# Optimization experiments

Measured on AMD Instinct MI355X. Metric: run time of the kernel, lower is better.

The kernel has to match this reference:

```python
import jax, jax.numpy as jnp
import numpy as np

H = 128  # hidden_dim
COORD_CLAMP = 100.0


def _glorot(key, shape):
    fan_in, fan_out = shape[0], shape[1]
    lim = float(np.sqrt(6.0 / (fan_in + fan_out)))
    return jax.random.uniform(key, shape, jnp.float32, -lim, lim)


def setup_inputs() -> dict:
    key = jax.random.key(0)
    ks = jax.random.split(key, 20)
    B, N = 2, 512
    inp = {
        "h": jax.random.normal(ks[0], (B, N, H), jnp.float32),
        "pos": jax.random.normal(ks[1], (B, N, 3), jnp.float32),
        "vel": jax.random.normal(ks[2], (B, N, 3), jnp.float32),
        # edge_mlp: Linear(2H+2 -> H), SiLU, Linear(H -> H), SiLU
        "We1": _glorot(ks[3], (2 * H + 2, H)), "be1": jnp.zeros((H,), jnp.float32),
        "We2": _glorot(ks[4], (H, H)), "be2": jnp.zeros((H,), jnp.float32),
        # attention_mlp: Linear(H -> 1), Sigmoid
        "Wa": _glorot(ks[5], (H, 1)), "ba": jnp.zeros((1,), jnp.float32),
        # pos_mlp: Linear(H -> H), SiLU, Linear(H -> 1, no bias)
        "Wp1": _glorot(ks[6], (H, H)), "bp1": jnp.zeros((H,), jnp.float32),
        "Wp2": _glorot(ks[7], (H, 1)),
        # vel_mlp: Linear(H -> H), SiLU, Linear(H -> 1, no bias)
        "Wv1": _glorot(ks[8], (H, H)), "bv1": jnp.zeros((H,), jnp.float32),
        "Wv2": _glorot(ks[9], (H, 1)),
        # node_mlp: Linear(2H -> H), SiLU, Linear(H -> H)
        "Wn1": _glorot(ks[10], (2 * H, H)), "bn1": jnp.zeros((H,), jnp.float32),
        "Wn2": _glorot(ks[11], (H, H)), "bn2": jnp.zeros((H,), jnp.float32),
    }
    return inp


def reference(h, pos, vel, We1, be1, We2, be2, Wa, ba,
              Wp1, bp1, Wp2, Wv1, bv1, Wv2, Wn1, bn1, Wn2, bn2):
    B, N, _ = pos.shape
    # pairwise diffs: [B, N, N, 3]
    pos_diff = pos[:, :, None, :] - pos[:, None, :, :]
    vel_diff = vel[:, :, None, :] - vel[:, None, :, :]
    pos_dist_sq = jnp.sum(pos_diff ** 2, axis=-1, keepdims=True)  # [B,N,N,1]
    vel_dist_sq = jnp.sum(vel_diff ** 2, axis=-1, keepdims=True)
    h_i = jnp.broadcast_to(h[:, :, None, :], (B, N, N, H))
    h_j = jnp.broadcast_to(h[:, None, :, :], (B, N, N, H))
    edge_input = jnp.concatenate([h_i, h_j, pos_dist_sq, vel_dist_sq], axis=-1)  # [B,N,N,2H+2]
    # edge MLP
    m = jax.nn.silu(jnp.einsum('bijc,ch->bijh', edge_input, We1) + be1)
    m_ij = jax.nn.silu(jnp.einsum('bijh,hk->bijk', m, We2) + be2)
    # attention gate
    att = jax.nn.sigmoid(jnp.einsum('bijh,ho->bijo', m_ij, Wa) + ba)  # [B,N,N,1]
    m_ij = m_ij * att
    # tanh-weighted coordinate/velocity updates
    pos_w = jnp.tanh(jnp.einsum('bijh,ho->bijo', jax.nn.silu(jnp.einsum('bijh,hk->bijk', m_ij, Wp1) + bp1), Wp2))
    vel_w = jnp.tanh(jnp.einsum('bijh,ho->bijo', jax.nn.silu(jnp.einsum('bijh,hk->bijk', m_ij, Wv1) + bv1), Wv2))
    denom = jnp.float32(max(N - 1, 1))
    pos_update = jnp.sum(pos_diff * pos_w, axis=2) / denom  # [B,N,3]
    vel_update = jnp.sum(vel_diff * vel_w, axis=2) / denom
    pos_out = jnp.clip(pos + pos_update, -COORD_CLAMP, COORD_CLAMP)
    vel_out = jnp.clip(vel + vel_update, -COORD_CLAMP, COORD_CLAMP)
    # node update
    m_agg = jnp.sum(m_ij, axis=2)  # [B,N,H]
    node_input = jnp.concatenate([h, m_agg], axis=-1)  # [B,N,2H]
    h_out = jax.nn.silu(jnp.einsum('bnc,ch->bnh', node_input, Wn1) + bn1)
    h_out = jnp.einsum('bnh,hk->bnk', h_out, Wn2) + bn2
    h_out = h + h_out  # residual
    return (h_out, pos_out, vel_out)
```

## Files before the change

kernel.cpp:

```cpp
#include <hip/hip_runtime.h>
#include <hip/hip_bf16.h>

#define Hd 128
#define Nn 512
#define TJ 32
#define LSTRIDE 136

typedef __bf16 bf16x8 __attribute__((ext_vector_type(8)));
typedef __bf16 bf16x4 __attribute__((ext_vector_type(4)));
typedef float  floatx4 __attribute__((ext_vector_type(4)));

__device__ __forceinline__ float frcp(float x){ return __builtin_amdgcn_rcpf(x); }
__device__ __forceinline__ float fsilu(float x){ return x * frcp(1.f + __expf(-x)); }
__device__ __forceinline__ float fsigm(float x){ return frcp(1.f + __expf(-x)); }
__device__ __forceinline__ float ftanh(float x){ return 1.f - 2.f * frcp(__expf(2.f*x) + 1.f); }
__device__ __forceinline__ float rfl(float x){
  return __int_as_float(__builtin_amdgcn_readfirstlane(__float_as_int(x)));
}

__global__ __launch_bounds__(256) void prep(const float* __restrict__ h,
                                            const float* __restrict__ We1,
                                            const float* __restrict__ be1,
                                            const float* __restrict__ We2,
                                            const float* __restrict__ Wp1,
                                            const float* __restrict__ Wv1,
                                            float* __restrict__ A,
                                            float* __restrict__ Bm,
                                            __bf16* __restrict__ dst,
                                            float* __restrict__ zbase){
  if (blockIdx.x < 256){
    const int r0 = blockIdx.x * 4;
    const int k = threadIdx.x & 127, ch = threadIdx.x >> 7;
    __shared__ float hL[4][Hd];
    __shared__ float pa[2][4][Hd], pb[2][4][Hd];
    for (int idx = threadIdx.x; idx < 4*Hd; idx += 256)
      hL[idx >> 7][idx & 127] = h[r0*Hd + idx];
    __syncthreads();
    float a[4] = {0.f,0.f,0.f,0.f}, bb[4] = {0.f,0.f,0.f,0.f};
    const int cbase = ch*64;
    #pragma unroll 4
    for (int cc = 0; cc < 64; ++cc){
      const int c = cbase + cc;
      const float wa = We1[c*Hd + k];
      const float wb = We1[(c + Hd)*Hd + k];
      #pragma unroll
      for (int rr = 0; rr < 4; ++rr){
        a[rr]  += hL[rr][c] * wa;
        bb[rr] += hL[rr][c] * wb;
      }
    }
    #pragma unroll
    for (int rr = 0; rr < 4; ++rr){ pa[ch][rr][k] = a[rr]; pb[ch][rr][k] = bb[rr]; }
    __syncthreads();
    if (threadIdx.x < Hd){
      const float be = be1[k];
      #pragma unroll
      for (int rr = 0; rr < 4; ++rr){
        A[(r0+rr)*Hd + k]  = pa[0][rr][k] + pa[1][rr][k] + be;
        Bm[(r0+rr)*Hd + k] = pb[0][rr][k] + pb[1][rr][k];
      }
    }
  } else if (blockIdx.x < 280){
    const int blk = blockIdx.x - 256;
    const int which = blk >> 3, m = blk & 7;
    const float* src = (which == 0) ? We2 : (which == 1 ? Wp1 : Wv1);
    __bf16* d = dst + which * (Hd*Hd);
    #pragma unroll
    for (int it = 0; it < 8; ++it){
      const int sidx = m*2048 + it*256 + threadIdx.x;
      const int kk = sidx >> 7, cc = sidx & 127;
      const int s = kk >> 5, j = kk & 7;
      const int lane = ((kk >> 3) & 3)*16 + (cc & 15);
      const int n = cc >> 4;
      d[n*2048 + s*512 + lane*8 + j] = (__bf16)src[sidx];
    }
  } else {
    const int t0 = (blockIdx.x - 280)*256 + threadIdx.x;
    for (int idx = t0; idx < 137216; idx += 2048) zbase[idx] = 0.f;
  }
}

__device__ __forceinline__ void gemm_kloopT(const __bf16* __restrict__ buf,
                                            const bf16x8* __restrict__ Ws,
                                            int w, int lane, int q, int l15,
                                            floatx4 acc[2][2]){
  const floatx4 zero = {0.f, 0.f, 0.f, 0.f};
  #pragma unroll
  for (int m = 0; m < 2; ++m){ acc[m][0] = zero; acc[m][1] = zero; }
  #pragma unroll
  for (int s = 0; s < 4; ++s){
    bf16x8 bf[2];
    #pragma unroll
    for (int n = 0; n < 2; ++n)
      bf[n] = *(const bf16x8*)&buf[(16*n + l15)*LSTRIDE + s*32 + q*8];
    const bf16x8 a0 = Ws[((2*w + 0)*4 + s)*64 + lane];
    const bf16x8 a1 = Ws[((2*w + 1)*4 + s)*64 + lane];
    #pragma unroll
    for (int n = 0; n < 2; ++n){
      acc[0][n] = __builtin_amdgcn_mfma_f32_16x16x32_bf16(a0, bf[n], acc[0][n], 0, 0, 0);
      acc[1][n] = __builtin_amdgcn_mfma_f32_16x16x32_bf16(a1, bf[n], acc[1][n], 0, 0, 0);
    }
  }
}

__device__ __forceinline__ void wdotT(floatx4 acc[2][2], float att0, float att1,
                                      const float* __restrict__ biasL,
                                      const float* __restrict__ w2L,
                                      int w, int lane, int q, int l15,
                                      float (*part)[TJ]){
  const int fb0 = 32*w + 4*q, fb1 = fb0 + 16;
  const floatx4 bb0 = *(const floatx4*)&biasL[fb0];
  const floatx4 bb1 = *(const floatx4*)&biasL[fb1];
  const floatx4 w0  = *(const floatx4*)&w2L[fb0];
  const floatx4 w1  = *(const floatx4*)&w2L[fb1];
  float p0 = 0.f, p1 = 0.f;
  #pragma unroll
  for (int r = 0; r < 4; ++r){
    p0 += fsilu(fmaf(att0, acc[0][0][r], bb0[r])) * w0[r];
    p0 += fsilu(fmaf(att0, acc[1][0][r], bb1[r])) * w1[r];
    p1 += fsilu(fmaf(att1, acc[0][1][r], bb0[r])) * w0[r];
    p1 += fsilu(fmaf(att1, acc[1][1][r], bb1[r])) * w1[r];
  }
  p0 += __shfl_xor(p0, 16, 64); p0 += __shfl_xor(p0, 32, 64);
  p1 += __shfl_xor(p1, 16, 64); p1 += __shfl_xor(p1, 32, 64);
  if (lane < 16){
    part[w][l15]      = p0;
    part[w][16 + l15] = p1;
  }
}

__global__ __launch_bounds__(256) void egnn_main(
    const float* __restrict__ pos, const float* __restrict__ vel,
    const float* __restrict__ We1, const float* __restrict__ be2,
    const float* __restrict__ Wa,  const float* __restrict__ ba,
    const float* __restrict__ bp1, const float* __restrict__ Wp2,
    const float* __restrict__ bv1, const float* __restrict__ Wv2,
    const float* __restrict__ A,   const float* __restrict__ Bm,
    const __bf16* __restrict__ Wsw,
    float* __restrict__ magg, float* __restrict__ posu, float* __restrict__ velu){

  const int t    = threadIdx.x;
  const int w    = t >> 6;
  const int lane = t & 63;
  const int q    = lane >> 4;
  const int l15  = lane & 15;
  const int node = blockIdx.x >> 1;
  const int half = blockIdx.x & 1;
  const int b    = node >> 9;

  __shared__ float AiL[Hd], wpL[Hd], wvL[Hd];
  __shared__ float be2L[Hd], bp1L[Hd], bv1L[Hd], WaL[Hd], Wp2L[Hd], Wv2L[Hd];
  __shared__ __align__(16) __bf16 bufm [TJ*LSTRIDE];
  __shared__ __align__(16) __bf16 bufij[TJ*LSTRIDE];
  __shared__ float partAtt[4][TJ], partP[4][TJ], partV[4][TJ];
  __shared__ float attL[TJ];

  if (t < Hd){
    AiL[t]  = A[node*Hd + t];
    wpL[t]  = We1[256*Hd + t];
    wvL[t]  = We1[257*Hd + t];
    be2L[t] = be2[t]; bp1L[t] = bp1[t]; bv1L[t] = bv1[t];
    WaL[t]  = Wa[t];  Wp2L[t] = Wp2[t]; Wv2L[t] = Wv2[t];
  }
  const float baV = ba[0];
  const float* pi = &pos[(size_t)node*3];
  const float* vi = &vel[(size_t)node*3];
  const float px = rfl(pi[0]), py = rfl(pi[1]), pz = rfl(pi[2]);
  const float ux = rfl(vi[0]), uy = rfl(vi[1]), uz = rfl(vi[2]);
  __syncthreads();

  const bf16x8* We2s = (const bf16x8*)(Wsw);
  const bf16x8* Wp1s = (const bf16x8*)(Wsw + Hd*Hd);
  const bf16x8* Wv1s = (const bf16x8*)(Wsw + 2*Hd*Hd);

  float accR[8];
  #pragma unroll
  for (int e = 0; e < 8; ++e) accR[e] = 0.f;

  for (int jt = 0; jt < (Nn/2)/TJ; ++jt){
    const int j0 = half*(Nn/2) + jt * TJ;

    {
      const int g  = t & 15;
      const int j2 = t >> 4;
      const floatx4 a0 = *(const floatx4*)&AiL[g*8];
      const floatx4 a1 = *(const floatx4*)&AiL[g*8 + 4];
      const floatx4 p0 = *(const floatx4*)&wpL[g*8];
      const floatx4 p1 = *(const floatx4*)&wpL[g*8 + 4];
      const floatx4 v0 = *(const floatx4*)&wvL[g*8];
      const floatx4 v1 = *(const floatx4*)&wvL[g*8 + 4];
      #pragma unroll
      for (int rr = 0; rr < 2; ++rr){
        const int j = j2 + rr*16;
        const int jg = j0 + j;
        const float* pj = &pos[(size_t)(b*Nn + jg)*3];
        const float* vj = &vel[(size_t)(b*Nn + jg)*3];
        const float dx = px - pj[0], dy = py - pj[1], dz = pz - pj[2];
        const float dp = dx*dx + dy*dy + dz*dz;
        const float ex = ux - vj[0], ey = uy - vj[1], ez = uz - vj[2];
        const float dv = ex*ex + ey*ey + ez*ez;
        const floatx4* Bp4 = (const floatx4*)&Bm[((size_t)(b*Nn + jg))*Hd + g*8];
        const floatx4 b0 = Bp4[0], b1 = Bp4[1];
        union { bf16x8 v; __hip_bfloat162 h2[4]; } o;
        float x[8];
        #pragma unroll
        for (int e = 0; e < 4; ++e){
          x[e]   = fsilu(a0[e] + b0[e] + dp*p0[e] + dv*v0[e]);
          x[4+e] = fsilu(a1[e] + b1[e] + dp*p1[e] + dv*v1[e]);
        }
        o.h2[0] = __float22bfloat162_rn(make_float2(x[0], x[1]));
        o.h2[1] = __float22bfloat162_rn(make_float2(x[2], x[3]));
        o.h2[2] = __float22bfloat162_rn(make_float2(x[4], x[5]));
        o.h2[3] = __float22bfloat162_rn(make_float2(x[6], x[7]));
        *(bf16x8*)&bufm[j*LSTRIDE + g*8] = o.v;
      }
    }
    __syncthreads();

    {
      floatx4 acc[2][2];
      gemm_kloopT(bufm, We2s, w, lane, q, l15, acc);
      const int fb0 = 32*w + 4*q, fb1 = fb0 + 16;
      const floatx4 be0 = *(const floatx4*)&be2L[fb0];
      const floatx4 be1 = *(const floatx4*)&be2L[fb1];
      const floatx4 wa0 = *(const floatx4*)&WaL[fb0];
      const floatx4 wa1 = *(const floatx4*)&WaL[fb1];
      float aw[2];
      #pragma unroll
      for (int n = 0; n < 2; ++n){
        const int j = 16*n + l15;
        float s0[4], s1[4];
        #pragma unroll
        for (int r = 0; r < 4; ++r){
          s0[r] = fsilu(acc[0][n][r] + be0[r]);
          s1[r] = fsilu(acc[1][n][r] + be1[r]);
        }
        aw[n] = s0[0]*wa0[0] + s0[1]*wa0[1] + s0[2]*wa0[2] + s0[3]*wa0[3]
              + s1[0]*wa1[0] + s1[1]*wa1[1] + s1[2]*wa1[2] + s1[3]*wa1[3];
        union { bf16x4 v; __hip_bfloat162 h2[2]; } p0k, p1k;
        p0k.h2[0] = __float22bfloat162_rn(make_float2(s0[0], s0[1]));
        p0k.h2[1] = __float22bfloat162_rn(make_float2(s0[2], s0[3]));
        p1k.h2[0] = __float22bfloat162_rn(make_float2(s1[0], s1[1]));
        p1k.h2[1] = __float22bfloat162_rn(make_float2(s1[2], s1[3]));
        *(bf16x4*)&bufij[j*LSTRIDE + fb0] = p0k.v;
        *(bf16x4*)&bufij[j*LSTRIDE + fb1] = p1k.v;
      }
      aw[0] += __shfl_xor(aw[0], 16, 64); aw[0] += __shfl_xor(aw[0], 32, 64);
      aw[1] += __shfl_xor(aw[1], 16, 64); aw[1] += __shfl_xor(aw[1], 32, 64);
      if (lane < 16){
        partAtt[w][l15]      = aw[0];
        partAtt[w][16 + l15] = aw[1];
      }
    }
    __syncthreads();

    {
      const float att0 = fsigm(partAtt[0][l15] + partAtt[1][l15] +
                               partAtt[2][l15] + partAtt[3][l15] + baV);
      const float att1 = fsigm(partAtt[0][16+l15] + partAtt[1][16+l15] +
                               partAtt[2][16+l15] + partAtt[3][16+l15] + baV);
      if (w == 0 && lane < 16){ attL[l15] = att0; attL[16 + l15] = att1; }
      floatx4 acc[2][2];
      gemm_kloopT(bufij, Wp1s, w, lane, q, l15, acc);
      wdotT(acc, att0, att1, bp1L, Wp2L, w, lane, q, l15, partP);
      gemm_kloopT(bufij, Wv1s, w, lane, q, l15, acc);
      wdotT(acc, att0, att1, bv1L, Wv2L, w, lane, q, l15, partV);
    }
    __syncthreads();

    if (w == 0){
      if (lane < TJ){
        const int jg = j0 + lane;
        const float* pj = &pos[(size_t)(b*Nn + jg)*3];
        const float s4 = partP[0][lane] + partP[1][lane] + partP[2][lane] + partP[3][lane];
        const float pw = ftanh(s4);
        accR[0] += (px - pj[0]) * pw;
        accR[1] += (py - pj[1]) * pw;
        accR[2] += (pz - pj[2]) * pw;
      }
    } else if (w == 1){
      if (lane < TJ){
        const int jg = j0 + lane;
        const float* vj = &vel[(size_t)(b*Nn + jg)*3];
        const float s4 = partV[0][lane] + partV[1][lane] + partV[2][lane] + partV[3][lane];
        const float vw = ftanh(s4);
        accR[0] += (ux - vj[0]) * vw;
        accR[1] += (uy - vj[1]) * vw;
        accR[2] += (uz - vj[2]) * vw;
      }
    } else {
      const int sg   = (w - 2)*8 + (lane & 7);
      const int jsub = lane >> 3;
      #pragma unroll
      for (int jj = 0; jj < 4; ++jj){
        const int j = jj*8 + jsub;
        const float aj = attL[j];
        const bf16x8 v = *(const bf16x8*)&bufij[j*LSTRIDE + sg*8];
        #pragma unroll
        for (int e = 0; e < 8; ++e) accR[e] += aj * (float)v[e];
      }
    }
  }

  if (w == 0 || w == 1){
    float v0 = accR[0], v1 = accR[1], v2 = accR[2];
    #pragma unroll
    for (int off = 1; off < 64; off <<= 1){
      v0 += __shfl_xor(v0, off, 64);
      v1 += __shfl_xor(v1, off, 64);
      v2 += __shfl_xor(v2, off, 64);
    }
    if (lane == 0){
      float* dst = (w == 0) ? &posu[node*3] : &velu[node*3];
      atomicAdd(&dst[0], v0);
      atomicAdd(&dst[1], v1);
      atomicAdd(&dst[2], v2);
    }
  } else {
    const int sg = (w - 2)*8 + (lane & 7);
    #pragma unroll
    for (int off = 8; off < 64; off <<= 1){
      #pragma unroll
      for (int e = 0; e < 8; ++e) accR[e] += __shfl_xor(accR[e], off, 64);
    }
    if ((lane >> 3) == 0){
      #pragma unroll
      for (int e = 0; e < 8; ++e)
        atomicAdd(&magg[node*Hd + sg*8 + e], accR[e]);
    }
  }
}

__global__ __launch_bounds__(256) void egnn_final(
    const float* __restrict__ h, const float* __restrict__ pos, const float* __restrict__ vel,
    const float* __restrict__ Wn1, const float* __restrict__ bn1,
    const float* __restrict__ Wn2, const float* __restrict__ bn2,
    const float* __restrict__ magg, const float* __restrict__ posu,
    const float* __restrict__ velu, float* __restrict__ out){
  const int row = blockIdx.x;
  const int t = threadIdx.x;
  const int k = t & 127, ch = t >> 7;
  __shared__ float ni[2*Hd];
  __shared__ float p1[2][Hd], t1[Hd];
  ni[t] = (t < Hd) ? h[row*Hd + t] : magg[row*Hd + (t - Hd)];
  __syncthreads();
  {
    float a0=0.f,a1=0.f,a2=0.f,a3=0.f;
    const int cb = ch*Hd;
    #pragma unroll 8
    for (int cc = 0; cc < Hd; cc += 4){
      a0 += ni[cb+cc+0] * Wn1[(cb+cc+0)*Hd + k];
      a1 += ni[cb+cc+1] * Wn1[(cb+cc+1)*Hd + k];
      a2 += ni[cb+cc+2] * Wn1[(cb+cc+2)*Hd + k];
      a3 += ni[cb+cc+3] * Wn1[(cb+cc+3)*Hd + k];
    }
    p1[ch][k] = (a0+a1)+(a2+a3);
  }
  __syncthreads();
  if (t < Hd) t1[t] = fsilu(p1[0][t] + p1[1][t] + bn1[t]);
  __syncthreads();
  {
    float a0=0.f,a1=0.f,a2=0.f,a3=0.f;
    const int cb = ch*64;
    #pragma unroll 8
    for (int cc = 0; cc < 64; cc += 4){
      a0 += t1[cb+cc+0] * Wn2[(cb+cc+0)*Hd + k];
      a1 += t1[cb+cc+1] * Wn2[(cb+cc+1)*Hd + k];
      a2 += t1[cb+cc+2] * Wn2[(cb+cc+2)*Hd + k];
      a3 += t1[cb+cc+3] * Wn2[(cb+cc+3)*Hd + k];
    }
    p1[ch][k] = (a0+a1)+(a2+a3);
  }
  __syncthreads();
  if (t < Hd){
    out[row*Hd + t] = ni[t] + p1[0][t] + p1[1][t] + bn2[t];
  } else if (t < Hd + 3){
    const int d = t - Hd;
    const float v = pos[row*3 + d] + posu[row*3 + d] * (1.f/511.f);
    out[2*Nn*Hd + row*3 + d] = fminf(fmaxf(v, -100.f), 100.f);
  } else if (t < Hd + 6){
    const int d = t - Hd - 3;
    const float v = vel[row*3 + d] + velu[row*3 + d] * (1.f/511.f);
    out[2*Nn*Hd + 2*Nn*3 + row*3 + d] = fminf(fmaxf(v, -100.f), 100.f);
  }
}

extern "C" void kernel_launch(void* const* d_in, const int* in_sizes, int n_in,
                              void* d_out, int out_size, void* d_ws, size_t ws_size,
                              hipStream_t stream){
  const float* h   = (const float*)d_in[0];
  const float* pos = (const float*)d_in[1];
  const float* vel = (const float*)d_in[2];
  const float* We1 = (const float*)d_in[3];
  const float* be1 = (const float*)d_in[4];
  const float* We2 = (const float*)d_in[5];
  const float* be2 = (const float*)d_in[6];
  const float* Wa  = (const float*)d_in[7];
  const float* ba  = (const float*)d_in[8];
  const float* Wp1 = (const float*)d_in[9];
  const float* bp1 = (const float*)d_in[10];
  const float* Wp2 = (const float*)d_in[11];
  const float* Wv1 = (const float*)d_in[12];
  const float* bv1 = (const float*)d_in[13];
  const float* Wv2 = (const float*)d_in[14];
  const float* Wn1 = (const float*)d_in[15];
  const float* bn1 = (const float*)d_in[16];
  const float* Wn2 = (const float*)d_in[17];
  const float* bn2 = (const float*)d_in[18];

  float* ws = (float*)d_ws;
  float*  A    = ws;
  float*  Bmm  = ws + 131072;
  float*  magg = ws + 262144;
  float*  posu = ws + 393216;
  float*  velu = ws + 396288;
  __bf16* Wsw  = (__bf16*)(ws + 399360);

  prep      <<<dim3(288),  dim3(256), 0, stream>>>(h, We1, be1, We2, Wp1, Wv1,
                                                   A, Bmm, Wsw, magg);
  egnn_main <<<dim3(2048), dim3(256), 0, stream>>>(pos, vel, We1, be2, Wa, ba, bp1, Wp2,
                                                   bv1, Wv2, A, Bmm, Wsw, magg, posu, velu);
  egnn_final<<<dim3(1024), dim3(256), 0, stream>>>(h, pos, vel, Wn1, bn1, Wn2, bn2,
                                                   magg, posu, velu, (float*)d_out);
}
```

Baseline: 233.4 us.

## Fuse prep, edge and node kernels into one cooperative kernel with grid sync

Replaces the three-kernel pipeline with a single cooperative kernel. Each block handles one node: it computes its own A/B projections and part of the weight swizzle, then runs a grid-wide sync. After that it processes all 512 neighbours instead of half, and performs the node MLP and the position and velocity outputs in place, with no global accumulation buffers. This removes two launches, the zero-fill, and the atomic or global round trips, but halves the grid to 1024 blocks (less parallelism) and adds a grid barrier. The old path stays as a fallback when occupancy is below 4 blocks per CU.

```diff
diff --git a/kernel.cpp b/kernel.cpp
--- a/kernel.cpp
+++ b/kernel.cpp
@@ -1,5 +1,8 @@
 #include <hip/hip_runtime.h>
 #include <hip/hip_bf16.h>
+#include <hip/hip_cooperative_groups.h>
+
+namespace cg = cooperative_groups;
 
 #define Hd 128
 #define Nn 512
@@ -16,68 +19,6 @@
 __device__ __forceinline__ float ftanh(float x){ return 1.f - 2.f * frcp(__expf(2.f*x) + 1.f); }
 __device__ __forceinline__ float rfl(float x){
   return __int_as_float(__builtin_amdgcn_readfirstlane(__float_as_int(x)));
-}
-
-__global__ __launch_bounds__(256) void prep(const float* __restrict__ h,
-                                            const float* __restrict__ We1,
-                                            const float* __restrict__ be1,
-                                            const float* __restrict__ We2,
-                                            const float* __restrict__ Wp1,
-                                            const float* __restrict__ Wv1,
-                                            float* __restrict__ A,
-                                            float* __restrict__ Bm,
-                                            __bf16* __restrict__ dst,
-                                            float* __restrict__ zbase){
-  if (blockIdx.x < 256){
-    const int r0 = blockIdx.x * 4;
-    const int k = threadIdx.x & 127, ch = threadIdx.x >> 7;
-    __shared__ float hL[4][Hd];
-    __shared__ float pa[2][4][Hd], pb[2][4][Hd];
-    for (int idx = threadIdx.x; idx < 4*Hd; idx += 256)
-      hL[idx >> 7][idx & 127] = h[r0*Hd + idx];
-    __syncthreads();
-    float a[4] = {0.f,0.f,0.f,0.f}, bb[4] = {0.f,0.f,0.f,0.f};
-    const int cbase = ch*64;
-    #pragma unroll 4
-    for (int cc = 0; cc < 64; ++cc){
-      const int c = cbase + cc;
-      const float wa = We1[c*Hd + k];
-      const float wb = We1[(c + Hd)*Hd + k];
-      #pragma unroll
-      for (int rr = 0; rr < 4; ++rr){
-        a[rr]  += hL[rr][c] * wa;
-        bb[rr] += hL[rr][c] * wb;
-      }
-    }
-    #pragma unroll
-    for (int rr = 0; rr < 4; ++rr){ pa[ch][rr][k] = a[rr]; pb[ch][rr][k] = bb[rr]; }
-    __syncthreads();
-    if (threadIdx.x < Hd){
-      const float be = be1[k];
-      #pragma unroll
-      for (int rr = 0; rr < 4; ++rr){
-        A[(r0+rr)*Hd + k]  = pa[0][rr][k] + pa[1][rr][k] + be;
-        Bm[(r0+rr)*Hd + k] = pb[0][rr][k] + pb[1][rr][k];
-      }
-    }
-  } else if (blockIdx.x < 280){
-    const int blk = blockIdx.x - 256;
-    const int which = blk >> 3, m = blk & 7;
-    const float* src = (which == 0) ? We2 : (which == 1 ? Wp1 : Wv1);
-    __bf16* d = dst + which * (Hd*Hd);
-    #pragma unroll
-    for (int it = 0; it < 8; ++it){
-      const int sidx = m*2048 + it*256 + threadIdx.x;
-      const int kk = sidx >> 7, cc = sidx & 127;
-      const int s = kk >> 5, j = kk & 7;
-      const int lane = ((kk >> 3) & 3)*16 + (cc & 15);
-      const int n = cc >> 4;
-      d[n*2048 + s*512 + lane*8 + j] = (__bf16)src[sidx];
-    }
-  } else {
-    const int t0 = (blockIdx.x - 280)*256 + threadIdx.x;
-    for (int idx = t0; idx < 137216; idx += 2048) zbase[idx] = 0.f;
-  }
 }
 
 __device__ __forceinline__ void gemm_kloopT(const __bf16* __restrict__ buf,
@@ -129,23 +70,27 @@
   }
 }
 
-__global__ __launch_bounds__(256) void egnn_main(
+__global__ __launch_bounds__(256) void egnn_coop(
+    const float* __restrict__ h,
     const float* __restrict__ pos, const float* __restrict__ vel,
-    const float* __restrict__ We1, const float* __restrict__ be2,
+    const float* __restrict__ We1, const float* __restrict__ be1,
+    const float* __restrict__ be2,
     const float* __restrict__ Wa,  const float* __restrict__ ba,
     const float* __restrict__ bp1, const float* __restrict__ Wp2,
     const float* __restrict__ bv1, const float* __restrict__ Wv2,
-    const float* __restrict__ A,   const float* __restrict__ Bm,
-    const __bf16* __restrict__ Wsw,
-    float* __restrict__ magg, float* __restrict__ posu, float* __restrict__ velu){
+    const float* __restrict__ Wn1, const float* __restrict__ bn1,
+    const float* __restrict__ Wn2, const float* __restrict__ bn2,
+    const float* __restrict__ We2, const float* __restrict__ Wp1,
+    const float* __restrict__ Wv1,
+    float* __restrict__ Bm, __bf16* __restrict__ Wsw,
+    float* __restrict__ out){
 
   const int t    = threadIdx.x;
   const int w    = t >> 6;
   const int lane = t & 63;
   const int q    = lane >> 4;
   const int l15  = lane & 15;
-  const int node = blockIdx.x >> 1;
-  const int half = blockIdx.x & 1;
+  const int node = blockIdx.x;
   const int b    = node >> 9;
 
   __shared__ float AiL[Hd], wpL[Hd], wvL[Hd];
@@ -155,8 +100,47 @@
   __shared__ float partAtt[4][TJ], partP[4][TJ], partV[4][TJ];
   __shared__ float attL[TJ];
 
+  {
+    const int k = t & 127, ch = t >> 7;
+    if (t < Hd) AiL[t] = h[(size_t)node*Hd + t];
+    __syncthreads();
+    float a = 0.f, bm = 0.f;
+    const int cb = ch*64;
+    #pragma unroll 4
+    for (int cc = 0; cc < 64; ++cc){
+      const int c = cb + cc;
+      const float hv = AiL[c];
+      a  += hv * We1[c*Hd + k];
+      bm += hv * We1[(c + Hd)*Hd + k];
+    }
+    float* pa = (float*)bufm;
+    float* pb = pa + 256;
+    pa[ch*128 + k] = a;
+    pb[ch*128 + k] = bm;
+    __syncthreads();
+    if (t < Hd){
+      const float av = pa[t] + pa[128 + t] + be1[t];
+      Bm[(size_t)node*Hd + t] = pb[t] + pb[128 + t];
+      AiL[t] = av;
+    }
+    if (node < 24){
+      const int which = node >> 3, m = node & 7;
+      const float* src = (which == 0) ? We2 : (which == 1 ? Wp1 : Wv1);
+      __bf16* d = Wsw + which * (Hd*Hd);
+      #pragma unroll
+      for (int it = 0; it < 8; ++it){
+        const int sidx = m*2048 + it*256 + t;
+        const int kk = sidx >> 7, cc2 = sidx & 127;
+        const int s = kk >> 5, j = kk & 7;
+        const int ln = ((kk >> 3) & 3)*16 + (cc2 & 15);
+        const int n = cc2 >> 4;
+        d[n*2048 + s*512 + ln*8 + j] = (__bf16)src[sidx];
+      }
+    }
+  }
+  cg::this_grid().sync();
+
   if (t < Hd){
-    AiL[t]  = A[node*Hd + t];
     wpL[t]  = We1[256*Hd + t];
     wvL[t]  = We1[257*Hd + t];
     be2L[t] = be2[t]; bp1L[t] = bp1[t]; bv1L[t] = bv1[t];
@@ -177,8 +161,8 @@
   #pragma unroll
   for (int e = 0; e < 8; ++e) accR[e] = 0.f;
 
-  for (int jt = 0; jt < (Nn/2)/TJ; ++jt){
-    const int j0 = half*(Nn/2) + jt * TJ;
+  for (int jt = 0; jt < Nn/TJ; ++jt){
+    const int j0 = jt * TJ;
 
     {
       const int g  = t & 15;
@@ -222,7 +206,7 @@
       gemm_kloopT(bufm, We2s, w, lane, q, l15, acc);
       const int fb0 = 32*w + 4*q, fb1 = fb0 + 16;
       const floatx4 be0 = *(const floatx4*)&be2L[fb0];
-      const floatx4 be1 = *(const floatx4*)&be2L[fb1];
+      const floatx4 be1v = *(const floatx4*)&be2L[fb1];
       const floatx4 wa0 = *(const floatx4*)&WaL[fb0];
       const floatx4 wa1 = *(const floatx4*)&WaL[fb1];
       float aw[2];
@@ -233,7 +217,7 @@
         #pragma unroll
         for (int r = 0; r < 4; ++r){
           s0[r] = fsilu(acc[0][n][r] + be0[r]);
-          s1[r] = fsilu(acc[1][n][r] + be1[r]);
+          s1[r] = fsilu(acc[1][n][r] + be1v[r]);
         }
         aw[n] = s0[0]*wa0[0] + s0[1]*wa0[1] + s0[2]*wa0[2] + s0[3]*wa0[3]
               + s1[0]*wa1[0] + s1[1]*wa1[1] + s1[2]*wa1[2] + s1[3]*wa1[3];
@@ -268,6 +252,310 @@
     }
     __syncthreads();
 
+    if (w == 0){
+      if (lane < TJ){
+        const int jg = j0 + lane;
+        const float* pj = &pos[(size_t)(b*Nn + jg)*3];
+        const float s4 = partP[0][lane] + partP[1][lane] + partP[2][lane] + partP[3][lane];
+        const float pw = ftanh(s4);
+        accR[0] += (px - pj[0]) * pw;
+        accR[1] += (py - pj[1]) * pw;
+        accR[2] += (pz - pj[2]) * pw;
+      }
+    } else if (w == 1){
+      if (lane < TJ){
+        const int jg = j0 + lane;
+        const float* vj = &vel[(size_t)(b*Nn + jg)*3];
+        const float s4 = partV[0][lane] + partV[1][lane] + partV[2][lane] + partV[3][lane];
+        const float vw = ftanh(s4);
+        accR[0] += (ux - vj[0]) * vw;
+        accR[1] += (uy - vj[1]) * vw;
+        accR[2] += (uz - vj[2]) * vw;
+      }
+    } else {
+      const int sg   = (w - 2)*8 + (lane & 7);
+      const int jsub = lane >> 3;
+      #pragma unroll
+      for (int jj = 0; jj < 4; ++jj){
+        const int j = jj*8 + jsub;
+        const float aj = attL[j];
+        const bf16x8 v = *(const bf16x8*)&bufij[j*LSTRIDE + sg*8];
+        #pragma unroll
+        for (int e = 0; e < 8; ++e) accR[e] += aj * (float)v[e];
+      }
+    }
+  }
+
+  float* sF = (float*)bufm;
+  if (t < Hd) sF[t] = h[(size_t)node*Hd + t];
+
+  if (w == 0 || w == 1){
+    float v0 = accR[0], v1 = accR[1], v2 = accR[2];
+    #pragma unroll
+    for (int off = 1; off < 64; off <<= 1){
+      v0 += __shfl_xor(v0, off, 64);
+      v1 += __shfl_xor(v1, off, 64);
+      v2 += __shfl_xor(v2, off, 64);
+    }
+    if (lane == 0){
+      const float inv = 1.f / 511.f;
+      if (w == 0){
+        float o0 = pi[0] + v0*inv, o1 = pi[1] + v1*inv, o2 = pi[2] + v2*inv;
+        out[2*Nn*Hd + node*3 + 0] = fminf(fmaxf(o0, -100.f), 100.f);
+        out[2*Nn*Hd + node*3 + 1] = fminf(fmaxf(o1, -100.f), 100.f);
+        out[2*Nn*Hd + node*3 + 2] = fminf(fmaxf(o2, -100.f), 100.f);
+      } else {
+        float o0 = vi[0] + v0*inv, o1 = vi[1] + v1*inv, o2 = vi[2] + v2*inv;
+        out[2*Nn*Hd + 2*Nn*3 + node*3 + 0] = fminf(fmaxf(o0, -100.f), 100.f);
+        out[2*Nn*Hd + 2*Nn*3 + node*3 + 1] = fminf(fmaxf(o1, -100.f), 100.f);
+        out[2*Nn*Hd + 2*Nn*3 + node*3 + 2] = fminf(fmaxf(o2, -100.f), 100.f);
+      }
+    }
+  } else {
+    const int sg = (w - 2)*8 + (lane & 7);
+    #pragma unroll
+    for (int off = 8; off < 64; off <<= 1){
+      #pragma unroll
+      for (int e = 0; e < 8; ++e) accR[e] += __shfl_xor(accR[e], off, 64);
+    }
+    if ((lane >> 3) == 0){
+      *(float4*)&sF[128 + sg*8 + 0] = make_float4(accR[0], accR[1], accR[2], accR[3]);
+      *(float4*)&sF[128 + sg*8 + 4] = make_float4(accR[4], accR[5], accR[6], accR[7]);
+    }
+  }
+  __syncthreads();
+
+  {
+    const int k = t & 127, ch = t >> 7;
+    const int cb = ch*Hd;
+    float a0=0.f,a1=0.f,a2=0.f,a3=0.f;
+    #pragma unroll 8
+    for (int cc = 0; cc < Hd; cc += 4){
+      a0 += sF[cb+cc+0] * Wn1[(cb+cc+0)*Hd + k];
+      a1 += sF[cb+cc+1] * Wn1[(cb+cc+1)*Hd + k];
+      a2 += sF[cb+cc+2] * Wn1[(cb+cc+2)*Hd + k];
+      a3 += sF[cb+cc+3] * Wn1[(cb+cc+3)*Hd + k];
+    }
+    sF[256 + ch*128 + k] = (a0+a1)+(a2+a3);
+  }
+  __syncthreads();
+  if (t < Hd) sF[512 + t] = fsilu(sF[256 + t] + sF[384 + t] + bn1[t]);
+  __syncthreads();
+  {
+    const int k = t & 127, ch = t >> 7;
+    const int cb = ch*64;
+    float a0=0.f,a1=0.f,a2=0.f,a3=0.f;
+    #pragma unroll 8
+    for (int cc = 0; cc < 64; cc += 4){
+      a0 += sF[512+cb+cc+0] * Wn2[(cb+cc+0)*Hd + k];
+      a1 += sF[512+cb+cc+1] * Wn2[(cb+cc+1)*Hd + k];
+      a2 += sF[512+cb+cc+2] * Wn2[(cb+cc+2)*Hd + k];
+      a3 += sF[512+cb+cc+3] * Wn2[(cb+cc+3)*Hd + k];
+    }
+    sF[256 + ch*128 + k] = (a0+a1)+(a2+a3);
+  }
+  __syncthreads();
+  if (t < Hd)
+    out[(size_t)node*Hd + t] = sF[t] + sF[256 + t] + sF[384 + t] + bn2[t];
+}
+
+__global__ __launch_bounds__(256) void prep(const float* __restrict__ h,
+                                            const float* __restrict__ We1,
+                                            const float* __restrict__ be1,
+                                            const float* __restrict__ We2,
+                                            const float* __restrict__ Wp1,
+                                            const float* __restrict__ Wv1,
+                                            float* __restrict__ A,
+                                            float* __restrict__ Bm,
+                                            __bf16* __restrict__ dst,
+                                            float* __restrict__ zbase){
+  if (blockIdx.x < 256){
+    const int r0 = blockIdx.x * 4;
+    const int k = threadIdx.x & 127, ch = threadIdx.x >> 7;
+    __shared__ float hL[4][Hd];
+    __shared__ float pa[2][4][Hd], pb[2][4][Hd];
+    for (int idx = threadIdx.x; idx < 4*Hd; idx += 256)
+      hL[idx >> 7][idx & 127] = h[r0*Hd + idx];
+    __syncthreads();
+    float a[4] = {0.f,0.f,0.f,0.f}, bb[4] = {0.f,0.f,0.f,0.f};
+    const int cbase = ch*64;
+    #pragma unroll 4
+    for (int cc = 0; cc < 64; ++cc){
+      const int c = cbase + cc;
+      const float wa = We1[c*Hd + k];
+      const float wb = We1[(c + Hd)*Hd + k];
+      #pragma unroll
+      for (int rr = 0; rr < 4; ++rr){
+        a[rr]  += hL[rr][c] * wa;
+        bb[rr] += hL[rr][c] * wb;
+      }
+    }
+    #pragma unroll
+    for (int rr = 0; rr < 4; ++rr){ pa[ch][rr][k] = a[rr]; pb[ch][rr][k] = bb[rr]; }
+    __syncthreads();
+    if (threadIdx.x < Hd){
+      const float be = be1[k];
+      #pragma unroll
+      for (int rr = 0; rr < 4; ++rr){
+        A[(r0+rr)*Hd + k]  = pa[0][rr][k] + pa[1][rr][k] + be;
+        Bm[(r0+rr)*Hd + k] = pb[0][rr][k] + pb[1][rr][k];
+      }
+    }
+  } else if (blockIdx.x < 280){
+    const int blk = blockIdx.x - 256;
+    const int which = blk >> 3, m = blk & 7;
+    const float* src = (which == 0) ? We2 : (which == 1 ? Wp1 : Wv1);
+    __bf16* d = dst + which * (Hd*Hd);
+    #pragma unroll
+    for (int it = 0; it < 8; ++it){
+      const int sidx = m*2048 + it*256 + threadIdx.x;
+      const int kk = sidx >> 7, cc = sidx & 127;
+      const int s = kk >> 5, j = kk & 7;
+      const int lane = ((kk >> 3) & 3)*16 + (cc & 15);
+      const int n = cc >> 4;
+      d[n*2048 + s*512 + lane*8 + j] = (__bf16)src[sidx];
+    }
+  } else {
+    const int t0 = (blockIdx.x - 280)*256 + threadIdx.x;
+    for (int idx = t0; idx < 137216; idx += 2048) zbase[idx] = 0.f;
+  }
+}
+
+__global__ __launch_bounds__(256) void egnn_main(
+    const float* __restrict__ pos, const float* __restrict__ vel,
+    const float* __restrict__ We1, const float* __restrict__ be2,
+    const float* __restrict__ Wa,  const float* __restrict__ ba,
+    const float* __restrict__ bp1, const float* __restrict__ Wp2,
+    const float* __restrict__ bv1, const float* __restrict__ Wv2,
+    const float* __restrict__ A,   const float* __restrict__ Bm,
+    const __bf16* __restrict__ Wsw,
+    float* __restrict__ magg, float* __restrict__ posu, float* __restrict__ velu){
+
+  const int t    = threadIdx.x;
+  const int w    = t >> 6;
+  const int lane = t & 63;
+  const int q    = lane >> 4;
+  const int l15  = lane & 15;
+  const int node = blockIdx.x >> 1;
+  const int half = blockIdx.x & 1;
+  const int b    = node >> 9;
+
+  __shared__ float AiL[Hd], wpL[Hd], wvL[Hd];
+  __shared__ float be2L[Hd], bp1L[Hd], bv1L[Hd], WaL[Hd], Wp2L[Hd], Wv2L[Hd];
+  __shared__ __align__(16) __bf16 bufm [TJ*LSTRIDE];
+  __shared__ __align__(16) __bf16 bufij[TJ*LSTRIDE];
+  __shared__ float partAtt[4][TJ], partP[4][TJ], partV[4][TJ];
+  __shared__ float attL[TJ];
+
+  if (t < Hd){
+    AiL[t]  = A[node*Hd + t];
+    wpL[t]  = We1[256*Hd + t];
+    wvL[t]  = We1[257*Hd + t];
+    be2L[t] = be2[t]; bp1L[t] = bp1[t]; bv1L[t] = bv1[t];
+    WaL[t]  = Wa[t];  Wp2L[t] = Wp2[t]; Wv2L[t] = Wv2[t];
+  }
+  const float baV = ba[0];
+  const float* pi = &pos[(size_t)node*3];
+  const float* vi = &vel[(size_t)node*3];
+  const float px = rfl(pi[0]), py = rfl(pi[1]), pz = rfl(pi[2]);
+  const float ux = rfl(vi[0]), uy = rfl(vi[1]), uz = rfl(vi[2]);
+  __syncthreads();
+
+  const bf16x8* We2s = (const bf16x8*)(Wsw);
+  const bf16x8* Wp1s = (const bf16x8*)(Wsw + Hd*Hd);
+  const bf16x8* Wv1s = (const bf16x8*)(Wsw + 2*Hd*Hd);
+
+  float accR[8];
+  #pragma unroll
+  for (int e = 0; e < 8; ++e) accR[e] = 0.f;
+
+  for (int jt = 0; jt < (Nn/2)/TJ; ++jt){
+    const int j0 = half*(Nn/2) + jt * TJ;
+    {
+      const int g  = t & 15;
+      const int j2 = t >> 4;
+      const floatx4 a0 = *(const floatx4*)&AiL[g*8];
+      const floatx4 a1 = *(const floatx4*)&AiL[g*8 + 4];
+      const floatx4 p0 = *(const floatx4*)&wpL[g*8];
+      const floatx4 p1 = *(const floatx4*)&wpL[g*8 + 4];
+      const floatx4 v0 = *(const floatx4*)&wvL[g*8];
+      const floatx4 v1 = *(const floatx4*)&wvL[g*8 + 4];
+      #pragma unroll
+      for (int rr = 0; rr < 2; ++rr){
+        const int j = j2 + rr*16;
+        const int jg = j0 + j;
+        const float* pj = &pos[(size_t)(b*Nn + jg)*3];
+        const float* vj = &vel[(size_t)(b*Nn + jg)*3];
+        const float dx = px - pj[0], dy = py - pj[1], dz = pz - pj[2];
+        const float dp = dx*dx + dy*dy + dz*dz;
+        const float ex = ux - vj[0], ey = uy - vj[1], ez = uz - vj[2];
+        const float dv = ex*ex + ey*ey + ez*ez;
+        const floatx4* Bp4 = (const floatx4*)&Bm[((size_t)(b*Nn + jg))*Hd + g*8];
+        const floatx4 b0 = Bp4[0], b1 = Bp4[1];
+        union { bf16x8 v; __hip_bfloat162 h2[4]; } o;
+        float x[8];
+        #pragma unroll
+        for (int e = 0; e < 4; ++e){
+          x[e]   = fsilu(a0[e] + b0[e] + dp*p0[e] + dv*v0[e]);
+          x[4+e] = fsilu(a1[e] + b1[e] + dp*p1[e] + dv*v1[e]);
+        }
+        o.h2[0] = __float22bfloat162_rn(make_float2(x[0], x[1]));
+        o.h2[1] = __float22bfloat162_rn(make_float2(x[2], x[3]));
+        o.h2[2] = __float22bfloat162_rn(make_float2(x[4], x[5]));
+        o.h2[3] = __float22bfloat162_rn(make_float2(x[6], x[7]));
+        *(bf16x8*)&bufm[j*LSTRIDE + g*8] = o.v;
+      }
+    }
+    __syncthreads();
+    {
+      floatx4 acc[2][2];
+      gemm_kloopT(bufm, We2s, w, lane, q, l15, acc);
+      const int fb0 = 32*w + 4*q, fb1 = fb0 + 16;
+      const floatx4 be0 = *(const floatx4*)&be2L[fb0];
+      const floatx4 be1v = *(const floatx4*)&be2L[fb1];
+      const floatx4 wa0 = *(const floatx4*)&WaL[fb0];
+      const floatx4 wa1 = *(const floatx4*)&WaL[fb1];
+      float aw[2];
+      #pragma unroll
+      for (int n = 0; n < 2; ++n){
+        const int j = 16*n + l15;
+        float s0[4], s1[4];
+        #pragma unroll
+        for (int r = 0; r < 4; ++r){
+          s0[r] = fsilu(acc[0][n][r] + be0[r]);
+          s1[r] = fsilu(acc[1][n][r] + be1v[r]);
+        }
+        aw[n] = s0[0]*wa0[0] + s0[1]*wa0[1] + s0[2]*wa0[2] + s0[3]*wa0[3]
+              + s1[0]*wa1[0] + s1[1]*wa1[1] + s1[2]*wa1[2] + s1[3]*wa1[3];
+        union { bf16x4 v; __hip_bfloat162 h2[2]; } p0k, p1k;
+        p0k.h2[0] = __float22bfloat162_rn(make_float2(s0[0], s0[1]));
+        p0k.h2[1] = __float22bfloat162_rn(make_float2(s0[2], s0[3]));
+        p1k.h2[0] = __float22bfloat162_rn(make_float2(s1[0], s1[1]));
+        p1k.h2[1] = __float22bfloat162_rn(make_float2(s1[2], s1[3]));
+        *(bf16x4*)&bufij[j*LSTRIDE + fb0] = p0k.v;
+        *(bf16x4*)&bufij[j*LSTRIDE + fb1] = p1k.v;
+      }
+      aw[0] += __shfl_xor(aw[0], 16, 64); aw[0] += __shfl_xor(aw[0], 32, 64);
+      aw[1] += __shfl_xor(aw[1], 16, 64); aw[1] += __shfl_xor(aw[1], 32, 64);
+      if (lane < 16){
+        partAtt[w][l15]      = aw[0];
+        partAtt[w][16 + l15] = aw[1];
+      }
+    }
+    __syncthreads();
+    {
+      const float att0 = fsigm(partAtt[0][l15] + partAtt[1][l15] +
+                               partAtt[2][l15] + partAtt[3][l15] + baV);
+      const float att1 = fsigm(partAtt[0][16+l15] + partAtt[1][16+l15] +
+                               partAtt[2][16+l15] + partAtt[3][16+l15] + baV);
+      if (w == 0 && lane < 16){ attL[l15] = att0; attL[16 + l15] = att1; }
+      floatx4 acc[2][2];
+      gemm_kloopT(bufij, Wp1s, w, lane, q, l15, acc);
+      wdotT(acc, att0, att1, bp1L, Wp2L, w, lane, q, l15, partP);
+      gemm_kloopT(bufij, Wv1s, w, lane, q, l15, acc);
+      wdotT(acc, att0, att1, bv1L, Wv2L, w, lane, q, l15, partV);
+    }
+    __syncthreads();
     if (w == 0){
       if (lane < TJ){
         const int jg = j0 + lane;
@@ -415,11 +703,29 @@
   float*  posu = ws + 393216;
   float*  velu = ws + 396288;
   __bf16* Wsw  = (__bf16*)(ws + 399360);
-
-  prep      <<<dim3(288),  dim3(256), 0, stream>>>(h, We1, be1, We2, Wp1, Wv1,
-                                                   A, Bmm, Wsw, magg);
-  egnn_main <<<dim3(2048), dim3(256), 0, stream>>>(pos, vel, We1, be2, Wa, ba, bp1, Wp2,
-                                                   bv1, Wv2, A, Bmm, Wsw, magg, posu, velu);
-  egnn_final<<<dim3(1024), dim3(256), 0, stream>>>(h, pos, vel, Wn1, bn1, Wn2, bn2,
-                                                   magg, posu, velu, (float*)d_out);
+  float*  outp = (float*)d_out;
+
+  int maxB = 0;
+  hipError_t qe = hipOccupancyMaxActiveBlocksPerMultiprocessor(
+      &maxB, (const void*)egnn_coop, 256, 0);
+  const bool coop = (qe == hipSuccess && maxB >= 4);
+
+  if (coop){
+    void* args[] = {
+      (void*)&h, (void*)&pos, (void*)&vel, (void*)&We1, (void*)&be1,
+      (void*)&be2, (void*)&Wa, (void*)&ba, (void*)&bp1, (void*)&Wp2,
+      (void*)&bv1, (void*)&Wv2, (void*)&Wn1, (void*)&bn1, (void*)&Wn2,
+      (void*)&bn2, (void*)&We2, (void*)&Wp1, (void*)&Wv1,
+      (void*)&Bmm, (void*)&Wsw, (void*)&outp
+    };
+    hipLaunchCooperativeKernel((const void*)egnn_coop, dim3(1024), dim3(256),
+                               args, 0, stream);
+  } else {
+    prep      <<<dim3(288),  dim3(256), 0, stream>>>(h, We1, be1, We2, Wp1, Wv1,
+                                                     A, Bmm, Wsw, magg);
+    egnn_main <<<dim3(2048), dim3(256), 0, stream>>>(pos, vel, We1, be2, Wa, ba, bp1, Wp2,
+                                                     bv1, Wv2, A, Bmm, Wsw, magg, posu, velu);
+    egnn_final<<<dim3(1024), dim3(256), 0, stream>>>(h, pos, vel, Wn1, bn1, Wn2, bn2,
+                                                     magg, posu, velu, outp);
+  }
 }
```

Result: no change. 232.1 us (-0.6%).
